# Optimization experiments

Hardware: AMD Instinct MI355X
Metric: run time of the kernel (lower is better)

The kernel has to match this reference:

```python
import jax, jax.numpy as jnp
import numpy as np

NEG_SLOPE_GAT = 0.2   # GATConv internal leaky_relu slope (PyG default)
NEG_SLOPE = 0.01      # nn.LeakyReLU default slope


def _gat(h_src_in, h_dst_in, src, dst, Wsrc, Wdst, a_s, a_d, b, n_dst, self_loops):
    """Single-head PyG-style GATConv: gather -> score -> edge softmax -> scatter-sum."""
    hs = h_src_in @ Wsrc            # [N_src, C]
    hd = h_dst_in @ Wdst            # [N_dst, C]
    if self_loops:                  # static flag; same node set on both sides
        loop = jnp.arange(n_dst, dtype=src.dtype)
        src = jnp.concatenate([src, loop])
        dst = jnp.concatenate([dst, loop])
    # attention logits per edge
    e = jax.nn.leaky_relu((hs @ a_s)[src] + (hd @ a_d)[dst], NEG_SLOPE_GAT)  # [E]
    # softmax over edges sharing a destination node
    m = jax.ops.segment_max(e, dst, num_segments=n_dst)
    ex = jnp.exp(e - m[dst])
    denom = jax.ops.segment_sum(ex, dst, num_segments=n_dst)
    alpha = ex / denom[dst]
    out = jax.ops.segment_sum(hs[src] * alpha[:, None], dst, num_segments=n_dst)
    return out + b


def setup_inputs() -> dict:
    key = jax.random.key(0)
    ks = iter(jax.random.split(key, 64))
    NB, NP = 100_000, 50_000
    E_bb, E_pp, E_bp = 800_000, 400_000, 400_000
    FB, FP, H, H2 = 32, 34, 64, 32
    rn = lambda shape, s=0.05: jax.random.normal(next(ks), shape, jnp.float32) * s
    d = {}
    d['x_b'] = rn((NB, FB), 1.0)
    d['x_p'] = rn((NP, FP), 1.0)
    d['ei_bb'] = jax.random.randint(next(ks), (2, E_bb), 0, NB, jnp.int32)
    d['ei_pp'] = jax.random.randint(next(ks), (2, E_pp), 0, NP, jnp.int32)
    d['ei_bp_src'] = jax.random.randint(next(ks), (E_bp,), 0, NB, jnp.int32)
    d['ei_bp_dst'] = jax.random.randint(next(ks), (E_bp,), 0, NP, jnp.int32)
    d['W_in_b'] = rn((FB, H)); d['b_in_b'] = jnp.zeros((H,), jnp.float32)
    d['W_in_p'] = rn((FP, H)); d['b_in_p'] = jnp.zeros((H,), jnp.float32)
    for tag, cin, cout in (('1', H, H), ('2', H, H2)):
        d['W_bb' + tag] = rn((cin, cout)); d['as_bb' + tag] = rn((cout,)); d['ad_bb' + tag] = rn((cout,)); d['b_bb' + tag] = jnp.zeros((cout,), jnp.float32)
        d['W_pp' + tag] = rn((cin, cout)); d['as_pp' + tag] = rn((cout,)); d['ad_pp' + tag] = rn((cout,)); d['b_pp' + tag] = jnp.zeros((cout,), jnp.float32)
        d['Ws_bp' + tag] = rn((cin, cout)); d['Wd_bp' + tag] = rn((cin, cout)); d['as_bp' + tag] = rn((cout,)); d['ad_bp' + tag] = rn((cout,)); d['b_bp' + tag] = jnp.zeros((cout,), jnp.float32)
    d['W_out'] = rn((H2, 1)); d['b_out'] = jnp.zeros((1,), jnp.float32)
    return d


def reference(x_b, x_p, ei_bb, ei_pp, ei_bp_src, ei_bp_dst,
              W_in_b, b_in_b, W_in_p, b_in_p,
              W_bb1, as_bb1, ad_bb1, b_bb1, W_pp1, as_pp1, ad_pp1, b_pp1,
              Ws_bp1, Wd_bp1, as_bp1, ad_bp1, b_bp1,
              W_bb2, as_bb2, ad_bb2, b_bb2, W_pp2, as_pp2, ad_pp2, b_pp2,
              Ws_bp2, Wd_bp2, as_bp2, ad_bp2, b_bp2,
              W_out, b_out):
    NB, NP = x_b.shape[0], x_p.shape[0]
    lr = lambda v: jax.nn.leaky_relu(v, NEG_SLOPE)
    # input projections (dropout is eval-mode identity)
    hb = lr(x_b @ W_in_b + b_in_b)
    hp = lr(x_p @ W_in_p + b_in_p)
    # hetero conv 1 (sum aggregation over relations sharing a dst type)
    ob = _gat(hb, hb, ei_bb[0], ei_bb[1], W_bb1, W_bb1, as_bb1, ad_bb1, b_bb1, NB, True)
    op = (_gat(hp, hp, ei_pp[0], ei_pp[1], W_pp1, W_pp1, as_pp1, ad_pp1, b_pp1, NP, True)
          + _gat(hb, hp, ei_bp_src, ei_bp_dst, Ws_bp1, Wd_bp1, as_bp1, ad_bp1, b_bp1, NP, False))
    hb, hp = lr(ob), lr(op)
    # hetero conv 2
    ob2 = _gat(hb, hb, ei_bb[0], ei_bb[1], W_bb2, W_bb2, as_bb2, ad_bb2, b_bb2, NB, True)
    op2 = (_gat(hp, hp, ei_pp[0], ei_pp[1], W_pp2, W_pp2, as_pp2, ad_pp2, b_pp2, NP, True)
           + _gat(hb, hp, ei_bp_src, ei_bp_dst, Ws_bp2, Wd_bp2, as_bp2, ad_bp2, b_bp2, NP, False))
    hp = lr(op2)
    return hp @ W_out + b_out  # [NP, 1]
```

## Files before the change

kernel.cpp:

```cpp
#include <hip/hip_runtime.h>
#include <hip/hip_bf16.h>
#include <cstdint>
#include <cstddef>


typedef __attribute__((ext_vector_type(8))) short short8;
typedef __attribute__((ext_vector_type(4))) float f32x4;
typedef unsigned int u32;
typedef __hip_bfloat16 bf16;

#define ABITS 9
#define CHUNKE 8192

static __device__ __forceinline__ float ldf(const void* p, int i, int bf) {
    return bf ? __bfloat162float(((const bf16*)p)[i]) : ((const float*)p)[i];
}

static __device__ __forceinline__ short f2bs(float f) {
    bf16 h = __float2bfloat16(f);
    return *reinterpret_cast<short*>(&h);
}
static __device__ __forceinline__ float bs2f(short s) {
    bf16 h = *reinterpret_cast<bf16*>(&s);
    return __bfloat162float(h);
}
static __device__ __forceinline__ float lo16(u32 u) { return bs2f((short)(u & 0xffffu)); }
static __device__ __forceinline__ float hi16(u32 u) { return bs2f((short)(u >> 16)); }
static __device__ __forceinline__ u32 pack2(float x, float y) {
    return (u32)(unsigned short)f2bs(x) | ((u32)(unsigned short)f2bs(y) << 16);
}
static __device__ __forceinline__ float sel4(const float* a, int i) {
    return i == 0 ? a[0] : i == 1 ? a[1] : i == 2 ? a[2] : a[3];
}
static __device__ __forceinline__ float lrelu2(float x) { return x > 0.f ? x : 0.2f * x; }

static __device__ __forceinline__ int probe_bf(const unsigned* __restrict__ w, int* cnt) {
    if (threadIdx.x == 0) *cnt = 0;
    __syncthreads();
    int c = 0;
#pragma unroll
    for (int j = 0; j < 4; ++j) {
        unsigned u = w[threadIdx.x * 4 + j];
        unsigned e = (u >> 7) & 0xffu;
        c += (e >= 100u && e <= 145u) ? 1 : 0;
    }
    atomicAdd(cnt, c);
    __syncthreads();
    int r = (*cnt > 614) ? 1 : 0;
    __syncthreads();
    return r;
}

__global__ __launch_bounds__(256) void k_fv_hist(
    const unsigned* __restrict__ probe_w, int* __restrict__ flag,
    const void* W_bb1, const void* as_bb1, const void* ad_bb1,
    const void* Ws_bp1, const void* as_bp1,
    const void* W_pp1, const void* as_pp1, const void* ad_pp1,
    const void* Wd_bp1, const void* ad_bp1,
    float* __restrict__ FVg,
    const int* __restrict__ bb_d, const int* __restrict__ pp_d,
    const int* __restrict__ bp_d, int* __restrict__ histM,
    int E_bb, int E_pp, int E_bp, int NB, int NP, int nbkt, int nblk)
{
    __shared__ int aux[1 << ABITS];
    if (blockIdx.x == 0) {
        int bf = probe_bf(probe_w, &aux[0]);
        if (threadIdx.x == 0) *flag = bf;
        int lane = threadIdx.x & 63, wv = threadIdx.x >> 6;
        const void* Ws[6] = { W_bb1, W_bb1, Ws_bp1, W_pp1, W_pp1, Wd_bp1 };
        const void* av[6] = { as_bb1, ad_bb1, as_bp1, as_pp1, ad_pp1, ad_bp1 };
#pragma unroll
        for (int v = 0; v < 6; ++v) {
            float a = ldf(av[v], lane, bf);
            for (int k = wv; k < 64; k += 4) {
                float p = ldf(Ws[v], k * 64 + lane, bf) * a;
#pragma unroll
                for (int off = 1; off < 64; off <<= 1) p += __shfl_xor(p, off);
                if (lane == 0) FVg[v * 64 + k] = p;
            }
        }
        return;
    }
    int blk = blockIdx.x - 1;
    for (int i = threadIdx.x; i < nbkt; i += 256) aux[i] = 0;
    __syncthreads();
    int E_all = E_bb + E_pp + E_bp;
    int base = blk * CHUNKE;
    int end = base + CHUNKE < E_all ? base + CHUNKE : E_all;
    for (int i = base + threadIdx.x; i < end; i += 256) {
        int d;
        if (i < E_bb) d = bb_d[i];
        else if (i < E_bb + E_pp) d = NB + pp_d[i - E_bb];
        else d = NB + NP + bp_d[i - E_bb - E_pp];
        atomicAdd(&aux[d >> ABITS], 1);
    }
    __syncthreads();
    for (int i = threadIdx.x; i < nbkt; i += 256)
        histM[(size_t)i * nblk + blk] = aux[i];
}

__global__ __launch_bounds__(1024) void k_scan1(const int* __restrict__ deg,
                                                int* __restrict__ out,
                                                int* __restrict__ bsum, int n)
{
    __shared__ int wsum[16];
    int gid = blockIdx.x * 1024 + threadIdx.x;
    int lane = threadIdx.x & 63, wid = threadIdx.x >> 6;
    int v = (gid < n) ? deg[gid] : 0;
    int x = v;
#pragma unroll
    for (int off = 1; off < 64; off <<= 1) {
        int y = __shfl_up(x, off, 64);
        if (lane >= off) x += y;
    }
    if (lane == 63) wsum[wid] = x;
    __syncthreads();
    if (wid == 0 && lane < 16) {
        int w0 = wsum[lane];
#pragma unroll
        for (int off = 1; off < 16; off <<= 1) {
            int y = __shfl_up(w0, off, 16);
            if (lane >= off) w0 += y;
        }
        wsum[lane] = w0;
    }
    __syncthreads();
    int base = (wid > 0) ? wsum[wid - 1] : 0;
    int incl = base + x;
    if (gid < n) out[gid] = incl - v;
    if (threadIdx.x == 1023) bsum[blockIdx.x] = incl;
}

__global__ __launch_bounds__(1024) void k_scan2(int* __restrict__ bsum, int nb)
{
    __shared__ int wsum[16];
    int lane = threadIdx.x & 63, wid = threadIdx.x >> 6;
    int v = (threadIdx.x < nb) ? bsum[threadIdx.x] : 0;
    int x = v;
#pragma unroll
    for (int off = 1; off < 64; off <<= 1) {
        int y = __shfl_up(x, off, 64);
        if (lane >= off) x += y;
    }
    if (lane == 63) wsum[wid] = x;
    __syncthreads();
    if (wid == 0 && lane < 16) {
        int w0 = wsum[lane];
#pragma unroll
        for (int off = 1; off < 16; off <<= 1) {
            int y = __shfl_up(w0, off, 16);
            if (lane >= off) w0 += y;
        }
        wsum[lane] = w0;
    }
    __syncthreads();
    int base = (wid > 0) ? wsum[wid - 1] : 0;
    if (threadIdx.x < nb) bsum[threadIdx.x] = base + x - v;
}

__global__ __launch_bounds__(1024) void k_scan3(int* __restrict__ indptr,
                                                const int* __restrict__ bsum,
                                                int n, int E)
{
    int gid = blockIdx.x * 1024 + threadIdx.x;
    if (gid < n) indptr[gid] += bsum[blockIdx.x];
    if (gid == 0) indptr[n] = E;
}

template <int CIN>
static __device__ __forceinline__ void in_proj_body(
    short* WT, float* bl, float* FV, int bid,
    const void* __restrict__ X, const void* __restrict__ W, const void* __restrict__ B,
    const float* __restrict__ FVg,
    bf16* __restrict__ Y,
    float* __restrict__ S0, float* __restrict__ S1v, float* __restrict__ S2v,
    int M, int bf)
{
    constexpr int KP = 40;
    for (int i = threadIdx.x; i < 64 * CIN; i += 256) {
        int n = i / CIN, k = i - n * CIN;
        WT[n * KP + k] = f2bs(ldf(W, k * 64 + n, bf));
    }
    if (threadIdx.x < 64) bl[threadIdx.x] = ldf(B, threadIdx.x, bf);
    if (threadIdx.x < 192) FV[threadIdx.x] = FVg[threadIdx.x];
    __syncthreads();

    int lane = threadIdx.x & 63;
    int wv   = threadIdx.x >> 6;
    int m = lane & 15, quad = lane >> 4;
    int row0 = (bid * 4 + wv) * 16;
    if (row0 >= M) return;

    int arow = row0 + m; if (arow >= M) arow = M - 1;
    short8 a;
#pragma unroll
    for (int j = 0; j < 8; ++j)
        a[j] = f2bs(ldf(X, arow * CIN + quad * 8 + j, bf));

    f32x4 acc[4] = {};
// ... 24 lines not shown

    float vs[4] = {}, vd[4] = {}, ve[4] = {};
#pragma unroll
    for (int tt = 0; tt < 4; ++tt) {
        int col = (lane & 15) + 16 * tt;
        float bb = bl[col];
        float w0 = FV[col], w1 = FV[64 + col], w2 = FV[128 + col];
#pragma unroll
        for (int r = 0; r < 4; ++r) {
            int row = row0 + quad * 4 + r;
            float v = acc[tt][r] + bb;
            v = v > 0.f ? v : 0.01f * v;
            if (row < M) Y[(size_t)row * 64 + col] = __float2bfloat16(v);
            vs[r] += v * w0; vd[r] += v * w1; ve[r] += v * w2;
        }
    }
#pragma unroll
    for (int off = 1; off < 16; off <<= 1)
#pragma unroll
        for (int r = 0; r < 4; ++r) {
            vs[r] += __shfl_xor(vs[r], off);
            vd[r] += __shfl_xor(vd[r], off);
            ve[r] += __shfl_xor(ve[r], off);
        }
    int c = lane & 15;
    int row = row0 + quad * 4 + (c & 3);
    if (row < M && c < 12) {
        if (c < 4)       S0[row]  = sel4(vs, c & 3);
        else if (c < 8)  S1v[row] = sel4(vd, c & 3);
        else             S2v[row] = sel4(ve, c & 3);
    }
}

__global__ __launch_bounds__(256) void k_scatter_inproj(
    const int* __restrict__ bb_s, const int* __restrict__ bb_d,
    const int* __restrict__ pp_s, const int* __restrict__ pp_d,
    const int* __restrict__ bp_s, const int* __restrict__ bp_d,
    const int* __restrict__ histS, unsigned* __restrict__ ebuf,
    int E_bb, int E_pp, int E_bp, int NB, int NP, int nbkt, int nblk,
    const void* __restrict__ Xb, const void* __restrict__ Wb, const void* __restrict__ Bb,
    bf16* __restrict__ Yb, int MB,
    const void* __restrict__ Xp, const void* __restrict__ Wp, const void* __restrict__ Bp,
    bf16* __restrict__ Yp, int MP,
    const float* __restrict__ FVg, const int* __restrict__ flag,
    float* __restrict__ ss_bb, float* __restrict__ sd_bb, float* __restrict__ ss_bp,
    float* __restrict__ ss_pp, float* __restrict__ sd_pp, float* __restrict__ sd_bp)
{
    __shared__ short WT[64 * 40];
    __shared__ float bl[64];
    __shared__ float FV[192];
    if ((int)blockIdx.x < nblk) {
        int* cur = (int*)WT;
        for (int i = threadIdx.x; i < nbkt; i += 256)
            cur[i] = histS[(size_t)i * nblk + blockIdx.x];
        __syncthreads();
        int E_all = E_bb + E_pp + E_bp;
        int base = blockIdx.x * CHUNKE;
        int end = base + CHUNKE < E_all ? base + CHUNKE : E_all;
        for (int i = base + threadIdx.x; i < end; i += 256) {
            int s, d;
            if (i < E_bb) { s = bb_s[i]; d = bb_d[i]; }
            else if (i < E_bb + E_pp) { int j = i - E_bb; s = pp_s[j]; d = NB + pp_d[j]; }
            else { int j = i - E_bb - E_pp; s = bp_s[j]; d = NB + NP + bp_d[j]; }
            int p = atomicAdd(&cur[d >> ABITS], 1);
            ebuf[p] = ((unsigned)(d & ((1 << ABITS) - 1)) << 20) | (unsigned)s;
        }
    } else {
        const int bfv = *flag;
        int bid = blockIdx.x - nblk;
        int nbb = (MB + 63) >> 6;
        if (bid < nbb)
            in_proj_body<32>(WT, bl, FV, bid, Xb, Wb, Bb, FVg,
                Yb, ss_bb, sd_bb, ss_bp, MB, bfv);
        else
            in_proj_body<34>(WT, bl, FV, bid - nbb, Xp, Wp, Bp, FVg + 192,
                Yp, ss_pp, sd_pp, sd_bp, MP, bfv);
    }
}

__global__ __launch_bounds__(256) void k_finalize(
    const unsigned* __restrict__ ebuf, const int* __restrict__ histS,
    int* __restrict__ ip_all, int2* __restrict__ sw,
    const float* __restrict__ ss_bb, const float* __restrict__ sd_bb,
    const float* __restrict__ ss_pp, const float* __restrict__ sd_pp,
    const float* __restrict__ ss_bp, const float* __restrict__ sd_bp,
    int NB, int NP, int NALL, int E_all, int nbkt, int nblk)
{
    __shared__ int h[1 << ABITS];
    __shared__ int pre[1 << ABITS];
    __shared__ int wq[4];
    int b = blockIdx.x;
    int d0 = b << ABITS;
    int nloc = NALL - d0 < (1 << ABITS) ? NALL - d0 : (1 << ABITS);
    int t = threadIdx.x;
    for (int i = t; i < (1 << ABITS); i += 256) h[i] = 0;
    __syncthreads();
    int s0 = histS[(size_t)b * nblk];
    int s1 = histS[(size_t)(b + 1) * nblk];
    for (int i = s0 + t; i < s1; i += 256)
        atomicAdd(&h[ebuf[i] >> 20], 1);
    __syncthreads();
    int v0 = h[2 * t], v1 = h[2 * t + 1];
    int ps = v0 + v1;
    int lane = t & 63, wid = t >> 6;
    int x = ps;
#pragma unroll
    for (int off = 1; off < 64; off <<= 1) {
        int y = __shfl_up(x, off, 64);
        if (lane >= off) x += y;
    }
    if (lane == 63) wq[wid] = x;
    __syncthreads();
    if (t == 0) {
        int a = 0;
#pragma unroll
        for (int w = 0; w < 4; ++w) { int tmp = wq[w]; wq[w] = a; a += tmp; }
    }
    __syncthreads();
    int excl = wq[wid] + x - ps;
    pre[2 * t]     = excl;
    pre[2 * t + 1] = excl + v0;
    __syncthreads();
    for (int i = t; i < nloc; i += 256) ip_all[d0 + i] = s0 + pre[i];
    if (d0 + nloc == NALL && t == 0) ip_all[NALL] = E_all;
    for (int i = t; i < (1 << ABITS); i += 256) h[i] = s0 + pre[i];
    __syncthreads();
    for (int i = s0 + t; i < s1; i += 256) {
        unsigned e = ebuf[i];
        int dl = (int)(e >> 20);
        int src = (int)(e & 0xFFFFFu);
        int p = atomicAdd(&h[dl], 1);
        int d = d0 + dl;
        float ssv, sdv;
        if (d < NB)           { ssv = ss_bb[src]; sdv = sd_bb[d]; }
        else if (d < NB + NP) { ssv = ss_pp[src]; sdv = sd_pp[d - NB]; }
        else                  { ssv = ss_bp[src]; sdv = sd_bp[d - NB - NP]; }
        int2 pk; pk.x = src; pk.y = __float_as_int(__expf(lrelu2(ssv + sdv)));
        sw[p] = pk;
    }
}

static __device__ __forceinline__ void gather1_body(
    int bid, const int* __restrict__ ip, const int2* __restrict__ sw,
    const float* __restrict__ SS, const float* __restrict__ SD,
    const bf16* __restrict__ HS, bf16* __restrict__ OUT, int M)
{
    int lane = threadIdx.x & 63;
    int half = lane >> 5, hl = lane & 31;
    int d = bid * 4 + (threadIdx.x >> 6);
    if (d >= M) return;
    const u32* H32 = (const u32*)HS;
    float ax = 0.f, ay = 0.f, den = 0.f;
    if (half == 0) {
        float ex = __expf(lrelu2(SS[d] + SD[d]));
        u32 h = H32[(size_t)d * 32 + hl];
        ax = lo16(h) * ex; ay = hi16(h) * ex; den = ex;
    }
    int j1 = ip[d + 1];
    int j = ip[d] + half;
    for (; j + 6 < j1; j += 8) {
        int2 p0 = sw[j], p1 = sw[j + 2], p2 = sw[j + 4], p3 = sw[j + 6];
        u32 h0 = H32[(size_t)p0.x * 32 + hl];
        u32 h1 = H32[(size_t)p1.x * 32 + hl];
        u32 h2 = H32[(size_t)p2.x * 32 + hl];
        u32 h3 = H32[(size_t)p3.x * 32 + hl];
        float e0 = __int_as_float(p0.y), e1 = __int_as_float(p1.y);
        float e2 = __int_as_float(p2.y), e3 = __int_as_float(p3.y);
        ax += lo16(h0) * e0 + lo16(h1) * e1 + lo16(h2) * e2 + lo16(h3) * e3;
        ay += hi16(h0) * e0 + hi16(h1) * e1 + hi16(h2) * e2 + hi16(h3) * e3;
        den += (e0 + e1) + (e2 + e3);
    }
    for (; j < j1; j += 2) {
        int2 p0 = sw[j];
        u32 h0 = H32[(size_t)p0.x * 32 + hl];
        float e0 = __int_as_float(p0.y);
        ax += lo16(h0) * e0; ay += hi16(h0) * e0; den += e0;
    }
    ax += __shfl_xor(ax, 32); ay += __shfl_xor(ay, 32); den += __shfl_xor(den, 32);
    if (half == 0) {
        float inv = 1.f / den;
        ((u32*)OUT)[(size_t)d * 32 + hl] = pack2(ax * inv, ay * inv);
    }
}

static __device__ __forceinline__ void gather2_body(
    int bid, const int* __restrict__ ip1, const int2* __restrict__ sw,
    const float* __restrict__ SS1, const float* __restrict__ SD1,
    const bf16* __restrict__ H1T,
    const int* __restrict__ ip2, const bf16* __restrict__ H2T,
    bf16* __restrict__ O1, bf16* __restrict__ O2, int M)
{
    int lane = threadIdx.x & 63;
    int half = lane >> 5, hl = lane & 31;
    int d = bid * 4 + (threadIdx.x >> 6);
    if (d >= M) return;
    const u32* H1 = (const u32*)H1T;
    const u32* H2 = (const u32*)H2T;
    float a1x = 0.f, a1y = 0.f, den1 = 0.f;
    if (half == 0) {
        float ex = __expf(lrelu2(SS1[d] + SD1[d]));
        u32 h = H1[(size_t)d * 32 + hl];
        a1x = lo16(h) * ex; a1y = hi16(h) * ex; den1 = ex;
    }
    int j1 = ip1[d + 1];
    int j = ip1[d] + half;
    for (; j + 6 < j1; j += 8) {
        int2 p0 = sw[j], p1 = sw[j + 2], p2 = sw[j + 4], p3 = sw[j + 6];
        u32 h0 = H1[(size_t)p0.x * 32 + hl];
        u32 h1 = H1[(size_t)p1.x * 32 + hl];
        u32 h2 = H1[(size_t)p2.x * 32 + hl];
        u32 h3 = H1[(size_t)p3.x * 32 + hl];
        float e0 = __int_as_float(p0.y), e1 = __int_as_float(p1.y);
        float e2 = __int_as_float(p2.y), e3 = __int_as_float(p3.y);
        a1x += lo16(h0) * e0 + lo16(h1) * e1 + lo16(h2) * e2 + lo16(h3) * e3;
        a1y += hi16(h0) * e0 + hi16(h1) * e1 + hi16(h2) * e2 + hi16(h3) * e3;
        den1 += (e0 + e1) + (e2 + e3);
    }
    for (; j < j1; j += 2) {
        int2 p0 = sw[j];
        u32 h0 = H1[(size_t)p0.x * 32 + hl];
        float e0 = __int_as_float(p0.y);
        a1x += lo16(h0) * e0; a1y += hi16(h0) * e0; den1 += e0;
    }
    float a2x = 0.f, a2y = 0.f, den2 = 0.f;
    j1 = ip2[d + 1];
    j = ip2[d] + half;
    for (; j + 6 < j1; j += 8) {
        int2 p0 = sw[j], p1 = sw[j + 2], p2 = sw[j + 4], p3 = sw[j + 6];
        u32 h0 = H2[(size_t)p0.x * 32 + hl];
        u32 h1 = H2[(size_t)p1.x * 32 + hl];
        u32 h2 = H2[(size_t)p2.x * 32 + hl];
        u32 h3 = H2[(size_t)p3.x * 32 + hl];
        float e0 = __int_as_float(p0.y), e1 = __int_as_float(p1.y);
        float e2 = __int_as_float(p2.y), e3 = __int_as_float(p3.y);
        a2x += lo16(h0) * e0 + lo16(h1) * e1 + lo16(h2) * e2 + lo16(h3) * e3;
        a2y += hi16(h0) * e0 + hi16(h1) * e1 + hi16(h2) * e2 + hi16(h3) * e3;
        den2 += (e0 + e1) + (e2 + e3);
    }
    for (; j < j1; j += 2) {
        int2 p0 = sw[j];
        u32 h0 = H2[(size_t)p0.x * 32 + hl];
        float e0 = __int_as_float(p0.y);
        a2x += lo16(h0) * e0; a2y += hi16(h0) * e0; den2 += e0;
    }
    a1x += __shfl_xor(a1x, 32); a1y += __shfl_xor(a1y, 32); den1 += __shfl_xor(den1, 32);
    a2x += __shfl_xor(a2x, 32); a2y += __shfl_xor(a2y, 32); den2 += __shfl_xor(den2, 32);
    if (half == 0) {
        float inv1 = 1.f / den1;
        float inv2 = den2 > 0.f ? 1.f / den2 : 0.f;
        ((u32*)O1)[(size_t)d * 32 + hl] = pack2(a1x * inv1, a1y * inv1);
        ((u32*)O2)[(size_t)d * 32 + hl] = pack2(a2x * inv2, a2y * inv2);
    }
}

__global__ __launch_bounds__(256) void k_gather12(
    const int* __restrict__ ip_bb, const int2* __restrict__ sw,
    const float* __restrict__ ss_bb, const float* __restrict__ sd_bb,
    const bf16* __restrict__ hb, bf16* __restrict__ agg_bb, int NB,
    const int* __restrict__ ip_pp, const int* __restrict__ ip_bp,
    const float* __restrict__ ss_pp, const float* __restrict__ sd_pp,
    const bf16* __restrict__ hp,
    bf16* __restrict__ agg_pp, bf16* __restrict__ agg_bp, int NP)
{
    int nbb = (NB + 3) >> 2;
    if ((int)blockIdx.x < nbb)
        gather1_body(blockIdx.x, ip_bb, sw, ss_bb, sd_bb, hb, agg_bb, NB);
    else
        gather2_body(blockIdx.x - nbb, ip_pp, sw, ss_pp, sd_pp, hp,
                     ip_bp, hb, agg_pp, agg_bp, NP);
}

template <bool D1, bool D2>
static __device__ __forceinline__ void fused_body(
    short* WT1, short* WT2, short* HT, float* bl, int bid,
    const bf16* __restrict__ A1, const bf16* __restrict__ A2,
    const void* W1a, const void* W1b, const void* B1a, const void* B1b,
    const void* W2a, const void* W2b,
    const void* av0, const void* av1, const void* av2,
    bf16* __restrict__ HS,
    float* __restrict__ S0, float* __restrict__ S1v, float* __restrict__ S2v,
    int M, int bf)
{
    constexpr int KP = 72;
    for (int i = threadIdx.x; i < 64 * 64; i += 256) {
        int n = i >> 6, k = i & 63;
        WT1[n * KP + k] = f2bs(ldf(W1a, k * 64 + n, bf));
        if (D1) WT1[(64 + n) * KP + k] = f2bs(ldf(W1b, k * 64 + n, bf));
    }
    for (int i = threadIdx.x; i < 32 * 64; i += 256) {
        int n = i >> 6, k = i & 63;
        WT2[n * KP + k] = f2bs(ldf(W2a, k * 32 + n, bf));
        if (D2) WT2[(32 + n) * KP + k] = f2bs(ldf(W2b, k * 32 + n, bf));
    }
    if (threadIdx.x < 64) {
        float b = ldf(B1a, threadIdx.x, bf);
        if (D1) b += ldf(B1b, threadIdx.x, bf);
        bl[threadIdx.x] = b;
    }
    __syncthreads();

    int lane = threadIdx.x & 63;
    int wv   = threadIdx.x >> 6;
// ... 104 lines not shown
}

__global__ __launch_bounds__(256) void k_fused_proj(
    const bf16* __restrict__ agg_pp, const bf16* __restrict__ agg_bp,
    const void* W_pp1, const void* Ws_bp1, const void* b_pp1, const void* b_bp1,
    const void* W_pp2, const void* Wd_bp2,
    const void* as_pp2, const void* ad_pp2, const void* ad_bp2,
    bf16* __restrict__ hs2_pp, float* __restrict__ ss2_pp,
    float* __restrict__ sd2_pp, float* __restrict__ sd2_bp, int MP,
    const bf16* __restrict__ agg_bb, const void* W_bb1, const void* b_bb1,
    const void* Ws_bp2, const void* as_bp2,
    bf16* __restrict__ hs2_bp, float* __restrict__ ss2_bp, int MB,
    const int* __restrict__ flag)
{
    const int bf = *flag;
    __shared__ __align__(16) short WT1[128 * 72];
    __shared__ __align__(16) short WT2[64 * 72];
    __shared__ __align__(16) short HT[64 * 80];
    __shared__ float bl[64];
    int npb = (MP + 63) >> 6;
    if ((int)blockIdx.x < npb)
        fused_body<true, true>(WT1, WT2, HT, bl, blockIdx.x,
            agg_pp, agg_bp, W_pp1, Ws_bp1, b_pp1, b_bp1,
            W_pp2, Wd_bp2, as_pp2, ad_pp2, ad_bp2,
            hs2_pp, ss2_pp, sd2_pp, sd2_bp, MP, bf);
    else
        fused_body<false, false>(WT1, WT2, HT, bl, blockIdx.x - npb,
            agg_bb, nullptr, W_bb1, nullptr, b_bb1, nullptr,
            Ws_bp2, nullptr, as_bp2, nullptr, nullptr,
            hs2_bp, ss2_bp, nullptr, nullptr, MB, bf);
}

__global__ __launch_bounds__(256) void k_gather_out(
    const int* __restrict__ ip1, const int2* __restrict__ sw,
    const float* __restrict__ SS1, const float* __restrict__ SD1,
    const bf16* __restrict__ HS1,
    const int* __restrict__ ip2,
    const float* __restrict__ SS2, const float* __restrict__ SD2,
    const bf16* __restrict__ HS2,
    const void* __restrict__ b1, const void* __restrict__ b2,
    const void* __restrict__ Wout, const void* __restrict__ bout,
    void* __restrict__ OUT, int M, const int* __restrict__ flag)
{
    const int bf = *flag;
    int lane = threadIdx.x & 63;
    int q = lane >> 4, hl = lane & 15;
    int d = blockIdx.x * 4 + (threadIdx.x >> 6);
    if (d >= M) return;
    const u32* H1 = (const u32*)HS1;
    const u32* H2 = (const u32*)HS2;
    float sdd = SD1[d];
    float a1x = 0.f, a1y = 0.f, den1 = 0.f;
    if (q == 0) {
        float ex = __expf(lrelu2(SS1[d] + sdd));
        u32 h = H1[(size_t)d * 16 + hl];
        a1x = lo16(h) * ex; a1y = hi16(h) * ex; den1 = ex;
    }
    int j1 = ip1[d + 1];
    int j = ip1[d] + q;
    for (; j + 4 < j1; j += 8) {
        int s0 = sw[j].x, s1 = sw[j + 4].x;
        u32 h0 = H1[(size_t)s0 * 16 + hl];
        u32 h1 = H1[(size_t)s1 * 16 + hl];
        float e0 = __expf(lrelu2(SS1[s0] + sdd));
        float e1 = __expf(lrelu2(SS1[s1] + sdd));
        a1x += lo16(h0) * e0 + lo16(h1) * e1;
        a1y += hi16(h0) * e0 + hi16(h1) * e1;
        den1 += e0 + e1;
    }
    if (j < j1) {
        int s0 = sw[j].x;
        u32 h0 = H1[(size_t)s0 * 16 + hl];
        float e0 = __expf(lrelu2(SS1[s0] + sdd));
        a1x += lo16(h0) * e0; a1y += hi16(h0) * e0; den1 += e0;
    }
    float sdd2 = SD2[d];
    float a2x = 0.f, a2y = 0.f, den2 = 0.f;
    j1 = ip2[d + 1];
    j = ip2[d] + q;
    for (; j + 4 < j1; j += 8) {
        int s0 = sw[j].x, s1 = sw[j + 4].x;
        u32 h0 = H2[(size_t)s0 * 16 + hl];
        u32 h1 = H2[(size_t)s1 * 16 + hl];
        float e0 = __expf(lrelu2(SS2[s0] + sdd2));
        float e1 = __expf(lrelu2(SS2[s1] + sdd2));
        a2x += lo16(h0) * e0 + lo16(h1) * e1;
        a2y += hi16(h0) * e0 + hi16(h1) * e1;
        den2 += e0 + e1;
    }
    if (j < j1) {
        int s0 = sw[j].x;
        u32 h0 = H2[(size_t)s0 * 16 + hl];
        float e0 = __expf(lrelu2(SS2[s0] + sdd2));
        a2x += lo16(h0) * e0; a2y += hi16(h0) * e0; den2 += e0;
    }
    a1x += __shfl_xor(a1x, 16); a1y += __shfl_xor(a1y, 16); den1 += __shfl_xor(den1, 16);
    a2x += __shfl_xor(a2x, 16); a2y += __shfl_xor(a2y, 16); den2 += __shfl_xor(den2, 16);
    a1x += __shfl_xor(a1x, 32); a1y += __shfl_xor(a1y, 32); den1 += __shfl_xor(den1, 32);
    a2x += __shfl_xor(a2x, 32); a2y += __shfl_xor(a2y, 32); den2 += __shfl_xor(den2, 32);
    float inv2 = den2 > 0.f ? 1.f / den2 : 0.f;
    float vx = a1x / den1 + a2x * inv2 + ldf(b1, 2 * hl, bf) + ldf(b2, 2 * hl, bf);
    float vy = a1y / den1 + a2y * inv2 + ldf(b1, 2 * hl + 1, bf) + ldf(b2, 2 * hl + 1, bf);
    vx = vx > 0.f ? vx : 0.01f * vx;
    vy = vy > 0.f ? vy : 0.01f * vy;
    float t = vx * ldf(Wout, 2 * hl, bf) + vy * ldf(Wout, 2 * hl + 1, bf);
#pragma unroll
    for (int off = 1; off < 16; off <<= 1) t += __shfl_xor(t, off);
    if (lane == 0) {
        float r = t + ldf(bout, 0, bf);
        if (bf) ((bf16*)OUT)[d] = __float2bfloat16(r);
        else    ((float*)OUT)[d] = r;
    }
}

extern "C" void kernel_launch(void* const* d_in, const int* in_sizes, int n_in,
                              void* d_out, int out_size, void* d_ws, size_t ws_size,
                              hipStream_t stream)
{
    const void* x_b = d_in[0];
    const void* x_p = d_in[1];
    const int* ei_bb = (const int*)d_in[2];
    const int* ei_pp = (const int*)d_in[3];
    const int* bp_s  = (const int*)d_in[4];
    const int* bp_d  = (const int*)d_in[5];
// ... 2 lines not shown
    const void *W_bb1 = d_in[10], *as_bb1 = d_in[11], *ad_bb1 = d_in[12], *b_bb1 = d_in[13];
    const void *W_pp1 = d_in[14], *as_pp1 = d_in[15], *ad_pp1 = d_in[16], *b_pp1 = d_in[17];
    const void *Ws_bp1 = d_in[18], *Wd_bp1 = d_in[19], *as_bp1 = d_in[20], *ad_bp1 = d_in[21], *b_bp1 = d_in[22];
    const void *W_pp2 = d_in[27], *as_pp2 = d_in[28], *ad_pp2 = d_in[29], *b_pp2 = d_in[30];
    const void *Ws_bp2 = d_in[31], *Wd_bp2 = d_in[32], *as_bp2 = d_in[33], *ad_bp2 = d_in[34], *b_bp2 = d_in[35];
    const void *W_out = d_in[36], *b_out = d_in[37];

    const int NB   = in_sizes[0] / 32;
    const int NP   = in_sizes[1] / 34;
    const int E_bb = in_sizes[2] / 2;
    const int E_pp = in_sizes[3] / 2;
    const int E_bp = in_sizes[4];
    const int E_all = E_bb + E_pp + E_bp;
    const int NALL  = NB + 2 * NP;
    const int* bb_s = ei_bb;  const int* bb_d = ei_bb + E_bb;
    const int* pp_s = ei_pp;  const int* pp_d = ei_pp + E_pp;
    (void)ws_size; (void)n_in; (void)out_size;

    const int nbkt  = (NALL + (1 << ABITS) - 1) >> ABITS;
    const int nblk  = (E_all + CHUNKE - 1) / CHUNKE;
    const int nh    = nbkt * nblk;

    char* base = (char*)d_ws;
    size_t o = 0;
    auto alloc = [&](size_t bytes) { char* p = base + o; o += (bytes + 255) & ~(size_t)255; return p; };

    int* flag  = (int*)alloc(256);
    float* FVg = (float*)alloc(6 * 64 * 4);
    int* bsum  = (int*)alloc(1024 * 4);
    int* histM = (int*)alloc((size_t)nh * 4);
    int* histS = (int*)alloc((size_t)(nh + 1) * 4);
    int* ip_all = (int*)alloc((size_t)(NALL + 1) * 4);
    unsigned* ebuf = (unsigned*)alloc((size_t)E_all * 4);
    int2* sw = (int2*)alloc((size_t)E_all * 8);
    float* ss_bb = (float*)alloc((size_t)NB * 4);
    float* sd_bb = (float*)alloc((size_t)NB * 4);
    float* ss_bp = (float*)alloc((size_t)NB * 4);
    float* ss_pp = (float*)alloc((size_t)NP * 4);
    float* sd_pp = (float*)alloc((size_t)NP * 4);
    float* sd_bp = (float*)alloc((size_t)NP * 4);
    float* ss2_bp = ss_bb;
    float* ss2_pp = ss_pp;
    float* sd2_pp = sd_pp;
    float* sd2_bp = sd_bp;

    char* S1 = alloc((size_t)NB * 64 * 2);
    char* S2 = alloc((size_t)NP * 64 * 2);
    char* S3 = alloc((size_t)NB * 64 * 2);
    char* S5 = alloc((size_t)NP * 64 * 2);
    char* S6 = alloc((size_t)NP * 64 * 2);

    bf16* hb     = (bf16*)S1;
    bf16* hp     = (bf16*)S2;
    bf16* agg_bb = (bf16*)S3;
    bf16* agg_bp = (bf16*)S5;
    bf16* agg_pp = (bf16*)S6;
    bf16* hs2_pp = (bf16*)S2;
    bf16* hs2_bp = (bf16*)S1;

    auto cdiv = [](int a, int b) { return (a + b - 1) / b; };

    const int* ip_bb = ip_all;
    const int* ip_pp = ip_all + NB;
    const int* ip_bp = ip_all + NB + NP;

    k_fv_hist<<<1 + nblk, 256, 0, stream>>>(
        (const unsigned*)x_b, flag,
        W_bb1, as_bb1, ad_bb1, Ws_bp1, as_bp1,
        W_pp1, as_pp1, ad_pp1, Wd_bp1, ad_bp1, FVg,
        bb_d, pp_d, bp_d, histM, E_bb, E_pp, E_bp, NB, NP, nbkt, nblk);

    int sb1 = cdiv(nh, 1024);
    k_scan1<<<sb1, 1024, 0, stream>>>(histM, histS, bsum, nh);
    k_scan2<<<1, 1024, 0, stream>>>(bsum, sb1);
    k_scan3<<<sb1, 1024, 0, stream>>>(histS, bsum, nh, E_all);

    k_scatter_inproj<<<nblk + cdiv(NB, 64) + cdiv(NP, 64), 256, 0, stream>>>(
        bb_s, bb_d, pp_s, pp_d, bp_s, bp_d, histS, ebuf,
        E_bb, E_pp, E_bp, NB, NP, nbkt, nblk,
        x_b, W_in_b, b_in_b, hb, NB, x_p, W_in_p, b_in_p, hp, NP,
        FVg, flag, ss_bb, sd_bb, ss_bp, ss_pp, sd_pp, sd_bp);

    k_finalize<<<nbkt, 256, 0, stream>>>(ebuf, histS, ip_all, sw,
                                         ss_bb, sd_bb, ss_pp, sd_pp, ss_bp, sd_bp,
                                         NB, NP, NALL, E_all, nbkt, nblk);

    k_gather12<<<cdiv(NB, 4) + cdiv(NP, 4), 256, 0, stream>>>(
        ip_bb, sw, ss_bb, sd_bb, hb, agg_bb, NB,
        ip_pp, ip_bp, ss_pp, sd_pp, hp, agg_pp, agg_bp, NP);

    k_fused_proj<<<cdiv(NP, 64) + cdiv(NB, 64), 256, 0, stream>>>(
        agg_pp, agg_bp, W_pp1, Ws_bp1, b_pp1, b_bp1,
        W_pp2, Wd_bp2, as_pp2, ad_pp2, ad_bp2,
        hs2_pp, ss2_pp, sd2_pp, sd2_bp, NP,
        agg_bb, W_bb1, b_bb1, Ws_bp2, as_bp2,
        hs2_bp, ss2_bp, NB, flag);

    k_gather_out<<<cdiv(NP, 4), 256, 0, stream>>>(
        ip_pp, sw, ss2_pp, sd2_pp, hs2_pp,
        ip_bp, ss2_bp, sd2_bp, hs2_bp,
        b_pp2, b_bp2, W_out, b_out, d_out, NP, flag);
}
```

Baseline: 405.4 us.

## Store only source indices per edge and recompute attention exp in gathers

```diff
diff --git a/kernel.cpp b/kernel.cpp
--- a/kernel.cpp
+++ b/kernel.cpp
@@ -51,120 +51,30 @@
     return r;
 }
 
-__global__ __launch_bounds__(256) void k_fv_hist(
+__global__ __launch_bounds__(256) void k_fv(
     const unsigned* __restrict__ probe_w, int* __restrict__ flag,
     const void* W_bb1, const void* as_bb1, const void* ad_bb1,
     const void* Ws_bp1, const void* as_bp1,
     const void* W_pp1, const void* as_pp1, const void* ad_pp1,
     const void* Wd_bp1, const void* ad_bp1,
-    float* __restrict__ FVg,
-    const int* __restrict__ bb_d, const int* __restrict__ pp_d,
-    const int* __restrict__ bp_d, int* __restrict__ histM,
-    int E_bb, int E_pp, int E_bp, int NB, int NP, int nbkt, int nblk)
-{
-    __shared__ int aux[1 << ABITS];
-    if (blockIdx.x == 0) {
-        int bf = probe_bf(probe_w, &aux[0]);
-        if (threadIdx.x == 0) *flag = bf;
-        int lane = threadIdx.x & 63, wv = threadIdx.x >> 6;
-        const void* Ws[6] = { W_bb1, W_bb1, Ws_bp1, W_pp1, W_pp1, Wd_bp1 };
-        const void* av[6] = { as_bb1, ad_bb1, as_bp1, as_pp1, ad_pp1, ad_bp1 };
-#pragma unroll
-        for (int v = 0; v < 6; ++v) {
-            float a = ldf(av[v], lane, bf);
-            for (int k = wv; k < 64; k += 4) {
-                float p = ldf(Ws[v], k * 64 + lane, bf) * a;
-#pragma unroll
-                for (int off = 1; off < 64; off <<= 1) p += __shfl_xor(p, off);
-                if (lane == 0) FVg[v * 64 + k] = p;
-            }
-        }
-        return;
-    }
-    int blk = blockIdx.x - 1;
-    for (int i = threadIdx.x; i < nbkt; i += 256) aux[i] = 0;
-    __syncthreads();
-    int E_all = E_bb + E_pp + E_bp;
-    int base = blk * CHUNKE;
-    int end = base + CHUNKE < E_all ? base + CHUNKE : E_all;
-    for (int i = base + threadIdx.x; i < end; i += 256) {
-        int d;
-        if (i < E_bb) d = bb_d[i];
-        else if (i < E_bb + E_pp) d = NB + pp_d[i - E_bb];
-        else d = NB + NP + bp_d[i - E_bb - E_pp];
-        atomicAdd(&aux[d >> ABITS], 1);
-    }
-    __syncthreads();
-    for (int i = threadIdx.x; i < nbkt; i += 256)
-        histM[(size_t)i * nblk + blk] = aux[i];
-}
-
-__global__ __launch_bounds__(1024) void k_scan1(const int* __restrict__ deg,
-                                                int* __restrict__ out,
-                                                int* __restrict__ bsum, int n)
-{
-    __shared__ int wsum[16];
-    int gid = blockIdx.x * 1024 + threadIdx.x;
-    int lane = threadIdx.x & 63, wid = threadIdx.x >> 6;
-    int v = (gid < n) ? deg[gid] : 0;
-    int x = v;
-#pragma unroll
-    for (int off = 1; off < 64; off <<= 1) {
-        int y = __shfl_up(x, off, 64);
-        if (lane >= off) x += y;
-    }
-    if (lane == 63) wsum[wid] = x;
-    __syncthreads();
-    if (wid == 0 && lane < 16) {
-        int w0 = wsum[lane];
-#pragma unroll
-        for (int off = 1; off < 16; off <<= 1) {
-            int y = __shfl_up(w0, off, 16);
-            if (lane >= off) w0 += y;
-        }
-        wsum[lane] = w0;
-    }
-    __syncthreads();
-    int base = (wid > 0) ? wsum[wid - 1] : 0;
-    int incl = base + x;
-    if (gid < n) out[gid] = incl - v;
-    if (threadIdx.x == 1023) bsum[blockIdx.x] = incl;
-}
-
-__global__ __launch_bounds__(1024) void k_scan2(int* __restrict__ bsum, int nb)
-{
-    __shared__ int wsum[16];
-    int lane = threadIdx.x & 63, wid = threadIdx.x >> 6;
-    int v = (threadIdx.x < nb) ? bsum[threadIdx.x] : 0;
-    int x = v;
-#pragma unroll
-    for (int off = 1; off < 64; off <<= 1) {
-        int y = __shfl_up(x, off, 64);
-        if (lane >= off) x += y;
-    }
-    if (lane == 63) wsum[wid] = x;
-    __syncthreads();
-    if (wid == 0 && lane < 16) {
-        int w0 = wsum[lane];
-#pragma unroll
-        for (int off = 1; off < 16; off <<= 1) {
-            int y = __shfl_up(w0, off, 16);
-            if (lane >= off) w0 += y;
-        }
-        wsum[lane] = w0;
-    }
-    __syncthreads();
-    int base = (wid > 0) ? wsum[wid - 1] : 0;
-    if (threadIdx.x < nb) bsum[threadIdx.x] = base + x - v;
-}
-
-__global__ __launch_bounds__(1024) void k_scan3(int* __restrict__ indptr,
-                                                const int* __restrict__ bsum,
-                                                int n, int E)
-{
-    int gid = blockIdx.x * 1024 + threadIdx.x;
-    if (gid < n) indptr[gid] += bsum[blockIdx.x];
-    if (gid == 0) indptr[n] = E;
+    float* __restrict__ FVg)
+{
+    __shared__ int cnt;
+    int bf = probe_bf(probe_w, &cnt);
+    if (threadIdx.x == 0) *flag = bf;
+    int lane = threadIdx.x & 63, wv = threadIdx.x >> 6;
+    const void* Ws[6] = { W_bb1, W_bb1, Ws_bp1, W_pp1, W_pp1, Wd_bp1 };
+    const void* av[6] = { as_bb1, ad_bb1, as_bp1, as_pp1, ad_pp1, ad_bp1 };
+#pragma unroll
+    for (int v = 0; v < 6; ++v) {
+        float a = ldf(av[v], lane, bf);
+        for (int k = wv; k < 64; k += 4) {
+            float p = ldf(Ws[v], k * 64 + lane, bf) * a;
+#pragma unroll
+            for (int off = 1; off < 64; off <<= 1) p += __shfl_xor(p, off);
+            if (lane == 0) FVg[v * 64 + k] = p;
+        }
+    }
 }
 
 template <int CIN>
@@ -255,7 +165,112 @@
     }
 }
 
-__global__ __launch_bounds__(256) void k_scatter_inproj(
+__global__ __launch_bounds__(256) void k_hist_projp(
+    const int* __restrict__ bb_d, const int* __restrict__ pp_d,
+    const int* __restrict__ bp_d, int* __restrict__ histM,
+    int E_bb, int E_pp, int E_bp, int NB, int NP, int nbkt, int nblk,
+    const void* __restrict__ Xp, const void* __restrict__ Wp, const void* __restrict__ Bp,
+    bf16* __restrict__ Yp, int MP,
+    const float* __restrict__ FVg, const int* __restrict__ flag,
+    float* __restrict__ ss_pp, float* __restrict__ sd_pp, float* __restrict__ sd_bp)
+{
+    __shared__ short WT[64 * 40];
+    __shared__ float bl[64];
+    __shared__ float FV[192];
+    __shared__ int aux[1 << ABITS];
+    if ((int)blockIdx.x < nblk) {
+        for (int i = threadIdx.x; i < nbkt; i += 256) aux[i] = 0;
+        __syncthreads();
+        int E_all = E_bb + E_pp + E_bp;
+        int base = blockIdx.x * CHUNKE;
+        int end = base + CHUNKE < E_all ? base + CHUNKE : E_all;
+        for (int i = base + threadIdx.x; i < end; i += 256) {
+            int d;
+            if (i < E_bb) d = bb_d[i];
+            else if (i < E_bb + E_pp) d = NB + pp_d[i - E_bb];
+            else d = NB + NP + bp_d[i - E_bb - E_pp];
+            atomicAdd(&aux[d >> ABITS], 1);
+        }
+        __syncthreads();
+        for (int i = threadIdx.x; i < nbkt; i += 256)
+            histM[(size_t)i * nblk + blockIdx.x] = aux[i];
+    } else {
+        const int bfv = *flag;
+        int bid = blockIdx.x - nblk;
+        in_proj_body<34>(WT, bl, FV, bid, Xp, Wp, Bp, FVg + 192,
+            Yp, ss_pp, sd_pp, sd_bp, MP, bfv);
+    }
+}
+
+__global__ __launch_bounds__(1024) void k_scan1(const int* __restrict__ deg,
+                                                int* __restrict__ out,
+                                                int* __restrict__ bsum, int n)
+{
+    __shared__ int wsum[16];
+    int gid = blockIdx.x * 1024 + threadIdx.x;
+    int lane = threadIdx.x & 63, wid = threadIdx.x >> 6;
+    int v = (gid < n) ? deg[gid] : 0;
+    int x = v;
+#pragma unroll
+    for (int off = 1; off < 64; off <<= 1) {
+        int y = __shfl_up(x, off, 64);
+        if (lane >= off) x += y;
+    }
+    if (lane == 63) wsum[wid] = x;
+    __syncthreads();
+    if (wid == 0 && lane < 16) {
+        int w0 = wsum[lane];
+#pragma unroll
+        for (int off = 1; off < 16; off <<= 1) {
+            int y = __shfl_up(w0, off, 16);
+            if (lane >= off) w0 += y;
+        }
+        wsum[lane] = w0;
+    }
+    __syncthreads();
+    int base = (wid > 0) ? wsum[wid - 1] : 0;
+    int incl = base + x;
+    if (gid < n) out[gid] = incl - v;
+    if (threadIdx.x == 1023) bsum[blockIdx.x] = incl;
+}
+
+__global__ __launch_bounds__(1024) void k_scan2(int* __restrict__ bsum, int nb)
+{
+    __shared__ int wsum[16];
+    int lane = threadIdx.x & 63, wid = threadIdx.x >> 6;
+    int v = (threadIdx.x < nb) ? bsum[threadIdx.x] : 0;
+    int x = v;
+#pragma unroll
+    for (int off = 1; off < 64; off <<= 1) {
+        int y = __shfl_up(x, off, 64);
+        if (lane >= off) x += y;
+    }
+    if (lane == 63) wsum[wid] = x;
+    __syncthreads();
+    if (wid == 0 && lane < 16) {
+        int w0 = wsum[lane];
+#pragma unroll
+        for (int off = 1; off < 16; off <<= 1) {
+            int y = __shfl_up(w0, off, 16);
+            if (lane >= off) w0 += y;
+        }
+        wsum[lane] = w0;
+    }
+    __syncthreads();
+    int base = (wid > 0) ? wsum[wid - 1] : 0;
+    if (threadIdx.x < nb) bsum[threadIdx.x] = base + x - v;
+}
+
+__global__ __launch_bounds__(1024) void k_scan3(int* __restrict__ indptr,
+                                                const int* __restrict__ bsum,
+                                                int n, int E)
+{
+    int gid = blockIdx.x * 1024 + threadIdx.x;
+    if (gid < n) indptr[gid] += bsum[blockIdx.x];
+    if (gid == 0) indptr[n] = E;
+}
+
+__global__ __launch_bounds__(256) void k_scatter_projb(
     const int* __restrict__ bb_s, const int* __restrict__ bb_d,
     const int* __restrict__ pp_s, const int* __restrict__ pp_d,
     const int* __restrict__ bp_s, const int* __restrict__ bp_d,
@@ -263,11 +278,8 @@
     int E_bb, int E_pp, int E_bp, int NB, int NP, int nbkt, int nblk,
     const void* __restrict__ Xb, const void* __restrict__ Wb, const void* __restrict__ Bb,
     bf16* __restrict__ Yb, int MB,
-    const void* __restrict__ Xp, const void* __restrict__ Wp, const void* __restrict__ Bp,
-    bf16* __restrict__ Yp, int MP,
     const float* __restrict__ FVg, const int* __restrict__ flag,
-    float* __restrict__ ss_bb, float* __restrict__ sd_bb, float* __restrict__ ss_bp,
-    float* __restrict__ ss_pp, float* __restrict__ sd_pp, float* __restrict__ sd_bp)
+    float* __restrict__ ss_bb, float* __restrict__ sd_bb, float* __restrict__ ss_bp)
 {
     __shared__ short WT[64 * 40];
     __shared__ float bl[64];
@@ -291,23 +303,15 @@
     } else {
         const int bfv = *flag;
         int bid = blockIdx.x - nblk;
-        int nbb = (MB + 63) >> 6;
-        if (bid < nbb)
-            in_proj_body<32>(WT, bl, FV, bid, Xb, Wb, Bb, FVg,
-                Yb, ss_bb, sd_bb, ss_bp, MB, bfv);
-        else
-            in_proj_body<34>(WT, bl, FV, bid - nbb, Xp, Wp, Bp, FVg + 192,
-                Yp, ss_pp, sd_pp, sd_bp, MP, bfv);
+        in_proj_body<32>(WT, bl, FV, bid, Xb, Wb, Bb, FVg,
+            Yb, ss_bb, sd_bb, ss_bp, MB, bfv);
     }
 }
 
 __global__ __launch_bounds__(256) void k_finalize(
     const unsigned* __restrict__ ebuf, const int* __restrict__ histS,
-    int* __restrict__ ip_all, int2* __restrict__ sw,
-    const float* __restrict__ ss_bb, const float* __restrict__ sd_bb,
-    const float* __restrict__ ss_pp, const float* __restrict__ sd_pp,
-    const float* __restrict__ ss_bp, const float* __restrict__ sd_bp,
-    int NB, int NP, int NALL, int E_all, int nbkt, int nblk)
+    int* __restrict__ ip_all, unsigned* __restrict__ sw2,
+    int NALL, int E_all, int nbkt, int nblk)
 {
     __shared__ int h[1 << ABITS];
     __shared__ int pre[1 << ABITS];
@@ -351,20 +355,13 @@
     for (int i = s0 + t; i < s1; i += 256) {
         unsigned e = ebuf[i];
         int dl = (int)(e >> 20);
-        int src = (int)(e & 0xFFFFFu);
         int p = atomicAdd(&h[dl], 1);
-        int d = d0 + dl;
-        float ssv, sdv;
-        if (d < NB)           { ssv = ss_bb[src]; sdv = sd_bb[d]; }
-        else if (d < NB + NP) { ssv = ss_pp[src]; sdv = sd_pp[d - NB]; }
-        else                  { ssv = ss_bp[src]; sdv = sd_bp[d - NB - NP]; }
-        int2 pk; pk.x = src; pk.y = __float_as_int(__expf(lrelu2(ssv + sdv)));
-        sw[p] = pk;
+        sw2[p] = e & 0xFFFFFu;
     }
 }
 
 static __device__ __forceinline__ void gather1_body(
-    int bid, const int* __restrict__ ip, const int2* __restrict__ sw,
+    int bid, const int* __restrict__ ip, const unsigned* __restrict__ sw2,
     const float* __restrict__ SS, const float* __restrict__ SD,
     const bf16* __restrict__ HS, bf16* __restrict__ OUT, int M)
 {
@@ -373,30 +370,34 @@
     int d = bid * 4 + (threadIdx.x >> 6);
     if (d >= M) return;
     const u32* H32 = (const u32*)HS;
+    float sdd = SD[d];
     float ax = 0.f, ay = 0.f, den = 0.f;
     if (half == 0) {
-        float ex = __expf(lrelu2(SS[d] + SD[d]));
+        float ex = __expf(lrelu2(SS[d] + sdd));
         u32 h = H32[(size_t)d * 32 + hl];
         ax = lo16(h) * ex; ay = hi16(h) * ex; den = ex;
     }
     int j1 = ip[d + 1];
     int j = ip[d] + half;
     for (; j + 6 < j1; j += 8) {
-        int2 p0 = sw[j], p1 = sw[j + 2], p2 = sw[j + 4], p3 = sw[j + 6];
-        u32 h0 = H32[(size_t)p0.x * 32 + hl];
-        u32 h1 = H32[(size_t)p1.x * 32 + hl];
-        u32 h2 = H32[(size_t)p2.x * 32 + hl];
-        u32 h3 = H32[(size_t)p3.x * 32 + hl];
-        float e0 = __int_as_float(p0.y), e1 = __int_as_float(p1.y);
-        float e2 = __int_as_float(p2.y), e3 = __int_as_float(p3.y);
+        int s0 = (int)sw2[j], s1 = (int)sw2[j + 2];
+        int s2 = (int)sw2[j + 4], s3 = (int)sw2[j + 6];
+        u32 h0 = H32[(size_t)s0 * 32 + hl];
+        u32 h1 = H32[(size_t)s1 * 32 + hl];
+        u32 h2 = H32[(size_t)s2 * 32 + hl];
+        u32 h3 = H32[(size_t)s3 * 32 + hl];
+        float e0 = __expf(lrelu2(SS[s0] + sdd));
+        float e1 = __expf(lrelu2(SS[s1] + sdd));
+        float e2 = __expf(lrelu2(SS[s2] + sdd));
+        float e3 = __expf(lrelu2(SS[s3] + sdd));
         ax += lo16(h0) * e0 + lo16(h1) * e1 + lo16(h2) * e2 + lo16(h3) * e3;
         ay += hi16(h0) * e0 + hi16(h1) * e1 + hi16(h2) * e2 + hi16(h3) * e3;
         den += (e0 + e1) + (e2 + e3);
     }
     for (; j < j1; j += 2) {
-        int2 p0 = sw[j];
-        u32 h0 = H32[(size_t)p0.x * 32 + hl];
-        float e0 = __int_as_float(p0.y);
+        int s0 = (int)sw2[j];
+        u32 h0 = H32[(size_t)s0 * 32 + hl];
+        float e0 = __expf(lrelu2(SS[s0] + sdd));
         ax += lo16(h0) * e0; ay += hi16(h0) * e0; den += e0;
     }
     ax += __shfl_xor(ax, 32); ay += __shfl_xor(ay, 32); den += __shfl_xor(den, 32);
@@ -407,10 +408,12 @@
 }
 
 static __device__ __forceinline__ void gather2_body(
-    int bid, const int* __restrict__ ip1, const int2* __restrict__ sw,
+    int bid, const int* __restrict__ ip1, const unsigned* __restrict__ sw2,
     const float* __restrict__ SS1, const float* __restrict__ SD1,
     const bf16* __restrict__ H1T,
-    const int* __restrict__ ip2, const bf16* __restrict__ H2T,
+    const int* __restrict__ ip2,
+    const float* __restrict__ SSb, const float* __restrict__ SDb,
+    const bf16* __restrict__ H2T,
     bf16* __restrict__ O1, bf16* __restrict__ O2, int M)
 {
     int lane = threadIdx.x & 63;
@@ -419,51 +422,59 @@
     if (d >= M) return;
     const u32* H1 = (const u32*)H1T;
     const u32* H2 = (const u32*)H2T;
+    float sdd1 = SD1[d];
     float a1x = 0.f, a1y = 0.f, den1 = 0.f;
     if (half == 0) {
-        float ex = __expf(lrelu2(SS1[d] + SD1[d]));
+        float ex = __expf(lrelu2(SS1[d] + sdd1));
         u32 h = H1[(size_t)d * 32 + hl];
         a1x = lo16(h) * ex; a1y = hi16(h) * ex; den1 = ex;
     }
     int j1 = ip1[d + 1];
     int j = ip1[d] + half;
     for (; j + 6 < j1; j += 8) {
-        int2 p0 = sw[j], p1 = sw[j + 2], p2 = sw[j + 4], p3 = sw[j + 6];
-        u32 h0 = H1[(size_t)p0.x * 32 + hl];
-        u32 h1 = H1[(size_t)p1.x * 32 + hl];
-        u32 h2 = H1[(size_t)p2.x * 32 + hl];
-        u32 h3 = H1[(size_t)p3.x * 32 + hl];
-        float e0 = __int_as_float(p0.y), e1 = __int_as_float(p1.y);
-        float e2 = __int_as_float(p2.y), e3 = __int_as_float(p3.y);
+        int s0 = (int)sw2[j], s1 = (int)sw2[j + 2];
+        int s2 = (int)sw2[j + 4], s3 = (int)sw2[j + 6];
+        u32 h0 = H1[(size_t)s0 * 32 + hl];
+        u32 h1 = H1[(size_t)s1 * 32 + hl];
+        u32 h2 = H1[(size_t)s2 * 32 + hl];
+        u32 h3 = H1[(size_t)s3 * 32 + hl];
+        float e0 = __expf(lrelu2(SS1[s0] + sdd1));
+        float e1 = __expf(lrelu2(SS1[s1] + sdd1));
+        float e2 = __expf(lrelu2(SS1[s2] + sdd1));
+        float e3 = __expf(lrelu2(SS1[s3] + sdd1));
         a1x += lo16(h0) * e0 + lo16(h1) * e1 + lo16(h2) * e2 + lo16(h3) * e3;
         a1y += hi16(h0) * e0 + hi16(h1) * e1 + hi16(h2) * e2 + hi16(h3) * e3;
         den1 += (e0 + e1) + (e2 + e3);
     }
     for (; j < j1; j += 2) {
-        int2 p0 = sw[j];
-        u32 h0 = H1[(size_t)p0.x * 32 + hl];
-        float e0 = __int_as_float(p0.y);
+        int s0 = (int)sw2[j];
+        u32 h0 = H1[(size_t)s0 * 32 + hl];
+        float e0 = __expf(lrelu2(SS1[s0] + sdd1));
         a1x += lo16(h0) * e0; a1y += hi16(h0) * e0; den1 += e0;
     }
+    float sdd2 = SDb[d];
     float a2x = 0.f, a2y = 0.f, den2 = 0.f;
     j1 = ip2[d + 1];
     j = ip2[d] + half;
     for (; j + 6 < j1; j += 8) {
-        int2 p0 = sw[j], p1 = sw[j + 2], p2 = sw[j + 4], p3 = sw[j + 6];
-        u32 h0 = H2[(size_t)p0.x * 32 + hl];
-        u32 h1 = H2[(size_t)p1.x * 32 + hl];
-        u32 h2 = H2[(size_t)p2.x * 32 + hl];
-        u32 h3 = H2[(size_t)p3.x * 32 + hl];
-        float e0 = __int_as_float(p0.y), e1 = __int_as_float(p1.y);
-        float e2 = __int_as_float(p2.y), e3 = __int_as_float(p3.y);
+        int s0 = (int)sw2[j], s1 = (int)sw2[j + 2];
+        int s2 = (int)sw2[j + 4], s3 = (int)sw2[j + 6];
+        u32 h0 = H2[(size_t)s0 * 32 + hl];
+        u32 h1 = H2[(size_t)s1 * 32 + hl];
+        u32 h2 = H2[(size_t)s2 * 32 + hl];
+        u32 h3 = H2[(size_t)s3 * 32 + hl];
+        float e0 = __expf(lrelu2(SSb[s0] + sdd2));
+        float e1 = __expf(lrelu2(SSb[s1] + sdd2));
+        float e2 = __expf(lrelu2(SSb[s2] + sdd2));
+        float e3 = __expf(lrelu2(SSb[s3] + sdd2));
         a2x += lo16(h0) * e0 + lo16(h1) * e1 + lo16(h2) * e2 + lo16(h3) * e3;
         a2y += hi16(h0) * e0 + hi16(h1) * e1 + hi16(h2) * e2 + hi16(h3) * e3;
         den2 += (e0 + e1) + (e2 + e3);
     }
     for (; j < j1; j += 2) {
-        int2 p0 = sw[j];
-        u32 h0 = H2[(size_t)p0.x * 32 + hl];
-        float e0 = __int_as_float(p0.y);
+        int s0 = (int)sw2[j];
+        u32 h0 = H2[(size_t)s0 * 32 + hl];
+        float e0 = __expf(lrelu2(SSb[s0] + sdd2));
         a2x += lo16(h0) * e0; a2y += hi16(h0) * e0; den2 += e0;
     }
     a1x += __shfl_xor(a1x, 32); a1y += __shfl_xor(a1y, 32); den1 += __shfl_xor(den1, 32);
@@ -477,20 +488,21 @@
 }
 
 __global__ __launch_bounds__(256) void k_gather12(
-    const int* __restrict__ ip_bb, const int2* __restrict__ sw,
+    const int* __restrict__ ip_bb, const unsigned* __restrict__ sw2,
     const float* __restrict__ ss_bb, const float* __restrict__ sd_bb,
     const bf16* __restrict__ hb, bf16* __restrict__ agg_bb, int NB,
     const int* __restrict__ ip_pp, const int* __restrict__ ip_bp,
     const float* __restrict__ ss_pp, const float* __restrict__ sd_pp,
+    const float* __restrict__ ss_bp, const float* __restrict__ sd_bp,
     const bf16* __restrict__ hp,
     bf16* __restrict__ agg_pp, bf16* __restrict__ agg_bp, int NP)
 {
     int nbb = (NB + 3) >> 2;
     if ((int)blockIdx.x < nbb)
-        gather1_body(blockIdx.x, ip_bb, sw, ss_bb, sd_bb, hb, agg_bb, NB);
+        gather1_body(blockIdx.x, ip_bb, sw2, ss_bb, sd_bb, hb, agg_bb, NB);
     else
-        gather2_body(blockIdx.x - nbb, ip_pp, sw, ss_pp, sd_pp, hp,
-                     ip_bp, hb, agg_pp, agg_bp, NP);
+        gather2_body(blockIdx.x - nbb, ip_pp, sw2, ss_pp, sd_pp, hp,
+                     ip_bp, ss_bp, sd_bp, hb, agg_pp, agg_bp, NP);
 }
 
 template <bool D1, bool D2>
@@ -661,7 +673,7 @@
 }
 
 __global__ __launch_bounds__(256) void k_gather_out(
-    const int* __restrict__ ip1, const int2* __restrict__ sw,
+    const int* __restrict__ ip1, const unsigned* __restrict__ sw2,
     const float* __restrict__ SS1, const float* __restrict__ SD1,
     const bf16* __restrict__ HS1,
     const int* __restrict__ ip2,
@@ -688,7 +700,7 @@
     int j1 = ip1[d + 1];
     int j = ip1[d] + q;
     for (; j + 4 < j1; j += 8) {
-        int s0 = sw[j].x, s1 = sw[j + 4].x;
+        int s0 = (int)sw2[j], s1 = (int)sw2[j + 4];
         u32 h0 = H1[(size_t)s0 * 16 + hl];
         u32 h1 = H1[(size_t)s1 * 16 + hl];
         float e0 = __expf(lrelu2(SS1[s0] + sdd));
@@ -698,7 +710,7 @@
         den1 += e0 + e1;
     }
     if (j < j1) {
-        int s0 = sw[j].x;
+        int s0 = (int)sw2[j];
         u32 h0 = H1[(size_t)s0 * 16 + hl];
         float e0 = __expf(lrelu2(SS1[s0] + sdd));
         a1x += lo16(h0) * e0; a1y += hi16(h0) * e0; den1 += e0;
@@ -708,7 +720,7 @@
     j1 = ip2[d + 1];
     j = ip2[d] + q;
     for (; j + 4 < j1; j += 8) {
-        int s0 = sw[j].x, s1 = sw[j + 4].x;
+        int s0 = (int)sw2[j], s1 = (int)sw2[j + 4];
         u32 h0 = H2[(size_t)s0 * 16 + hl];
         u32 h1 = H2[(size_t)s1 * 16 + hl];
         float e0 = __expf(lrelu2(SS2[s0] + sdd2));
@@ -718,7 +730,7 @@
         den2 += e0 + e1;
     }
     if (j < j1) {
-        int s0 = sw[j].x;
+        int s0 = (int)sw2[j];
         u32 h0 = H2[(size_t)s0 * 16 + hl];
         float e0 = __expf(lrelu2(SS2[s0] + sdd2));
         a2x += lo16(h0) * e0; a2y += hi16(h0) * e0; den2 += e0;
@@ -787,7 +799,7 @@
     int* histS = (int*)alloc((size_t)(nh + 1) * 4);
     int* ip_all = (int*)alloc((size_t)(NALL + 1) * 4);
     unsigned* ebuf = (unsigned*)alloc((size_t)E_all * 4);
-    int2* sw = (int2*)alloc((size_t)E_all * 8);
+    unsigned* sw2  = (unsigned*)alloc((size_t)E_all * 4);
     float* ss_bb = (float*)alloc((size_t)NB * 4);
     float* sd_bb = (float*)alloc((size_t)NB * 4);
     float* ss_bp = (float*)alloc((size_t)NB * 4);
@@ -819,30 +831,34 @@
     const int* ip_pp = ip_all + NB;
     const int* ip_bp = ip_all + NB + NP;
 
-    k_fv_hist<<<1 + nblk, 256, 0, stream>>>(
+    k_fv<<<1, 256, 0, stream>>>(
         (const unsigned*)x_b, flag,
         W_bb1, as_bb1, ad_bb1, Ws_bp1, as_bp1,
-        W_pp1, as_pp1, ad_pp1, Wd_bp1, ad_bp1, FVg,
-        bb_d, pp_d, bp_d, histM, E_bb, E_pp, E_bp, NB, NP, nbkt, nblk);
+        W_pp1, as_pp1, ad_pp1, Wd_bp1, ad_bp1, FVg);
+
+    k_hist_projp<<<nblk + cdiv(NP, 64), 256, 0, stream>>>(
+        bb_d, pp_d, bp_d, histM,
+        E_bb, E_pp, E_bp, NB, NP, nbkt, nblk,
+        x_p, W_in_p, b_in_p, hp, NP,
+        FVg, flag, ss_pp, sd_pp, sd_bp);
 
     int sb1 = cdiv(nh, 1024);
     k_scan1<<<sb1, 1024, 0, stream>>>(histM, histS, bsum, nh);
     k_scan2<<<1, 1024, 0, stream>>>(bsum, sb1);
     k_scan3<<<sb1, 1024, 0, stream>>>(histS, bsum, nh, E_all);
 
-    k_scatter_inproj<<<nblk + cdiv(NB, 64) + cdiv(NP, 64), 256, 0, stream>>>(
+    k_scatter_projb<<<nblk + cdiv(NB, 64), 256, 0, stream>>>(
         bb_s, bb_d, pp_s, pp_d, bp_s, bp_d, histS, ebuf,
         E_bb, E_pp, E_bp, NB, NP, nbkt, nblk,
-        x_b, W_in_b, b_in_b, hb, NB, x_p, W_in_p, b_in_p, hp, NP,
-        FVg, flag, ss_bb, sd_bb, ss_bp, ss_pp, sd_pp, sd_bp);
-
-    k_finalize<<<nbkt, 256, 0, stream>>>(ebuf, histS, ip_all, sw,
-                                         ss_bb, sd_bb, ss_pp, sd_pp, ss_bp, sd_bp,
-                                         NB, NP, NALL, E_all, nbkt, nblk);
+        x_b, W_in_b, b_in_b, hb, NB,
+        FVg, flag, ss_bb, sd_bb, ss_bp);
+
+    k_finalize<<<nbkt, 256, 0, stream>>>(ebuf, histS, ip_all, sw2,
+                                         NALL, E_all, nbkt, nblk);
 
     k_gather12<<<cdiv(NB, 4) + cdiv(NP, 4), 256, 0, stream>>>(
-        ip_bb, sw, ss_bb, sd_bb, hb, agg_bb, NB,
-        ip_pp, ip_bp, ss_pp, sd_pp, hp, agg_pp, agg_bp, NP);
+        ip_bb, sw2, ss_bb, sd_bb, hb, agg_bb, NB,
+        ip_pp, ip_bp, ss_pp, sd_pp, ss_bp, sd_bp, hp, agg_pp, agg_bp, NP);
 
     k_fused_proj<<<cdiv(NP, 64) + cdiv(NB, 64), 256, 0, stream>>>(
         agg_pp, agg_bp, W_pp1, Ws_bp1, b_pp1, b_bp1,
@@ -852,7 +868,7 @@
         hs2_bp, ss2_bp, NB, flag);
 
     k_gather_out<<<cdiv(NP, 4), 256, 0, stream>>>(
-        ip_pp, sw, ss2_pp, sd2_pp, hs2_pp,
+        ip_pp, sw2, ss2_pp, sd2_pp, hs2_pp,
         ip_bp, ss2_bp, sd2_bp, hs2_bp,
         b_pp2, b_bp2, W_out, b_out, d_out, NP, flag);
 }
```

Measured after the change: 406.6 us. No clear change (+0.3%).
